# Optimization experiments

Measured on AMD Instinct MI355X. Metric: run time of the kernel, lower is better.

The kernel has to match this reference:

```python
import jax, jax.numpy as jnp
import numpy as np

B, T, HID = 2, 2048, 1024
H, DK, DV = 8, 128, 128      # num_heads, head_f_dim (key), head_i_dim (value)
LR = 128                     # gate low-rank dim
EPS = 1e-5


def setup_inputs() -> dict:
    key = jax.random.key(0)
    ks = jax.random.split(key, 8)
    def w(k, shape, fan_in):
        return jax.random.normal(k, shape, jnp.float32) / np.float32(np.sqrt(fan_in))
    return {
        "hidden_states": jax.random.normal(ks[0], (B, T, HID), jnp.float32),
        "Wq": w(ks[1], (HID, HID), HID),   # key_dim x hidden
        "Wk": w(ks[2], (HID, HID), HID),
        "Wv": w(ks[3], (HID, HID), HID),   # value_dim x hidden
        "Wg1": w(ks[4], (LR, HID), HID),   # low-rank gate down
        "Wg2": w(ks[5], (HID, LR), LR),    # low-rank gate up
        "g_norm_weight": jnp.ones((HID,), jnp.float32),
        "Wo": w(ks[6], (HID, HID), HID),
    }


def _lightnet_fwd(x, Wq, Wk, Wv, Wg1, Wg2, g_norm_weight, Wo):
    b, t, _ = x.shape
    q = jax.nn.silu(x @ Wq.T).reshape(b, t, H, DK)
    k = (x @ Wk.T).reshape(b, t, H, DK)
    v = (x @ Wv.T).reshape(b, t, H, DV)

    # LightNet gating: normalized keys via logcumsumexp over time
    z = jax.lax.cumlogsumexp(k, axis=1)                 # [b,t,h,dk]
    k = jnp.exp(k - z)                                  # exp-normalized keys
    g = jnp.concatenate([z[:, :1], z[:, :-1]], axis=1) - z  # <= 0; g[:,0]=0

    scale = DK ** -0.5

    # gated linear attention recurrence: S_t = exp(g_t) * S_{t-1} + k_t v_t^T
    def step(S, inp):
        qt, kt, vt, gt = inp                            # [b,h,dk],[b,h,dk],[b,h,dv],[b,h,dk]
        S = jnp.exp(gt)[..., None] * S + kt[..., None] * vt[..., None, :]
        o = jnp.einsum('bhk,bhkv->bhv', qt, S) * scale
        return S, o

    S0 = jnp.zeros((b, H, DK, DV), x.dtype)
    tfirst = lambda a: jnp.moveaxis(a, 1, 0)
    _, oT = jax.lax.scan(step, S0, (tfirst(q), tfirst(k), tfirst(v), tfirst(g)))
    o = jnp.moveaxis(oT, 0, 1).reshape(b, t, H * DV)    # [b,t,hidden]

    # RMSNorm(o) * swish(gate) then output projection
    gate = (x @ Wg1.T) @ Wg2.T
    o = o * jax.lax.rsqrt(jnp.mean(o * o, axis=-1, keepdims=True) + EPS) * g_norm_weight
    o = o * gate * jax.nn.sigmoid(gate)
    return o @ Wo.T


def reference(hidden_states, Wq, Wk, Wv, Wg1, Wg2, g_norm_weight, Wo):
    return _lightnet_fwd(hidden_states, Wq, Wk, Wv, Wg1, Wg2, g_norm_weight, Wo)
```

## Files before the change

kernel.cpp:

```cpp
#include <hip/hip_runtime.h>
#include <hip/hip_bf16.h>
#include <stdint.h>


typedef short short8 __attribute__((ext_vector_type(8)));
typedef float f32x4 __attribute__((ext_vector_type(4)));

#define T_SEQ 2048
#define HIDN  1024
#define SCALE 0.08838834764831845f
#define LDSP  136

__device__ __forceinline__ float blo(unsigned int u){
  union{unsigned int i; float f;} v; v.i = u << 16; return v.f;
}
__device__ __forceinline__ float bhi(unsigned int u){
  union{unsigned int i; float f;} v; v.i = u & 0xffff0000u; return v.f;
}
__device__ __forceinline__ float bu2f(unsigned short u){
  union{unsigned int i; float f;} v; v.i = ((unsigned int)u) << 16; return v.f;
}
__device__ __forceinline__ unsigned short f2bu(float f){
  union{float f; unsigned int i;} v; v.f = f;
  unsigned int x = v.i;
  x += 0x7fffu + ((x >> 16) & 1u);
  return (unsigned short)(x >> 16);
}
__device__ __forceinline__ void async16(const void* g, void* l){
  __builtin_amdgcn_global_load_lds(
      (const __attribute__((address_space(1))) unsigned int*)g,
      (__attribute__((address_space(3))) unsigned int*)l, 16, 0, 0);
}

__global__ __launch_bounds__(256) void convert_all(
    const float* __restrict__ X,  const float* __restrict__ Wq,
    const float* __restrict__ Wk, const float* __restrict__ Wv,
    const float* __restrict__ Wg1,const float* __restrict__ Wg2,
    const float* __restrict__ gnw,const float* __restrict__ Wo,
    unsigned short* __restrict__ base, float* __restrict__ SumSq)
{
  int q = blockIdx.x * 256 + threadIdx.x;
  const float* src; unsigned short* dst; int rel = q;
  if (rel < 1048576)            { src = X;   dst = base;            }
  else if ((rel -= 1048576) < 262144) { src = Wq;  dst = base + 4194304; }
  else if ((rel -=  262144) < 262144) { src = Wk;  dst = base + 5242880; }
  else if ((rel -=  262144) < 262144) { src = Wv;  dst = base + 6291456; }
  else if ((rel -=  262144) < 262144) { src = Wo;  dst = base + 7340032; }
  else if ((rel -=  262144) <  32768) { src = Wg1; dst = base + 8388608; }
  else if ((rel -=   32768) <  32768) { src = Wg2; dst = base + 8519680; }
  else if ((rel -=   32768) <    256) { src = gnw; dst = base + 8650752; }
  else { rel -= 256;
    ((float4*)SumSq)[rel] = make_float4(0.f,0.f,0.f,0.f); return; }
  float4 v = ((const float4*)src)[rel];
  ushort4 o; o.x=f2bu(v.x); o.y=f2bu(v.y); o.z=f2bu(v.z); o.w=f2bu(v.w);
  ((ushort4*)dst)[rel] = o;
}

__device__ __forceinline__ void gemm_core(
    const unsigned short* __restrict__ A, const unsigned short* __restrict__ B,
    int K, int row0, int col0,
    unsigned short* sA, unsigned short* sB, f32x4 acc[4][4], int tid)
{
  const int lane = tid & 63;
  const int wm = (tid >> 6) & 1, wn = tid >> 7;
  const int wb = tid & 192;
  for (int k0 = 0; k0 < K; k0 += 64){
    __syncthreads();
#pragma unroll
    for (int r = 0; r < 4; ++r){
      int idx  = r*256 + tid;
      int mrow = idx >> 3;
      int kc   = ((idx & 7) ^ (mrow & 7)) * 8;
      async16(A + (size_t)(row0 + mrow)*K + k0 + kc,
              sA + (size_t)(r*256 + wb)*8);
      async16(B + (size_t)(col0 + mrow)*K + k0 + kc,
              sB + (size_t)(r*256 + wb)*8);
    }
    __syncthreads();
#pragma unroll
    for (int h = 0; h < 2; ++h){
      short8 av[4], bv[4];
#pragma unroll
      for (int i=0;i<4;i++){
        int ra = wm*64 + i*16 + (lane&15);
        av[i] = *(const short8*)(sA + (size_t)ra*64
                                 + (((h*4 + (lane>>4)) ^ (ra & 7)) * 8));
      }
#pragma unroll
      for (int j=0;j<4;j++){
        int rb = wn*64 + j*16 + (lane&15);
        bv[j] = *(const short8*)(sB + (size_t)rb*64
                                 + (((h*4 + (lane>>4)) ^ (rb & 7)) * 8));
      }
#pragma unroll
      for (int i=0;i<4;i++)
#pragma unroll
        for (int j=0;j<4;j++)
          acc[i][j] = __builtin_amdgcn_mfma_f32_16x16x32_bf16(av[i], bv[j], acc[i][j], 0, 0, 0);
    }
  }
}

__device__ __forceinline__ void epilogue_lds(
    f32x4 acc[4][4], int row0, int col0, int tid, int ldc, int act,
    unsigned short* __restrict__ Cb, unsigned short* sC)
{
  const int lane = tid & 63;
  const int wm = (tid >> 6) & 1, wn = tid >> 7;
#pragma unroll
  for (int p=0;p<4;p++){
    __syncthreads();
    if (wm == (p>>1)){
#pragma unroll
      for (int ii=0; ii<2; ii++){
        int i = (p&1)*2 + ii;
        int lr = i*16 + ((lane>>4)<<2) - (p&1)*32;
#pragma unroll
        for (int j=0;j<4;j++){
          int col = wn*64 + j*16 + (lane&15);
#pragma unroll
          for (int r=0;r<4;r++){
            float v = acc[i][j][r];
            if (act == 1) v = v / (1.f + __expf(-v));
            else if (act == 2) v = __expf(v);
            sC[(lr+r)*128 + col] = f2bu(v);
          }
        }
      }
    }
    __syncthreads();
#pragma unroll
    for (int c = tid; c < 512; c += 256){
      int rr = c >> 4, off = (c & 15)*8;
      *(uint4*)&Cb[(size_t)(row0 + p*32 + rr)*ldc + col0 + off] =
          *(const uint4*)&sC[rr*128 + off];
    }
  }
}

__device__ __forceinline__ void epilogue_f32(
    f32x4 acc[4][4], int row0, int col0, int tid, int ldc,
    float* __restrict__ Cf)
{
  const int lane = tid & 63;
  const int wm = (tid >> 6) & 1, wn = tid >> 7;
#pragma unroll
  for (int i=0;i<4;i++){
    int rbase = row0 + wm*64 + i*16 + ((lane>>4)<<2);
#pragma unroll
    for (int j=0;j<4;j++){
      int col = col0 + wn*64 + j*16 + (lane&15);
#pragma unroll
      for (int r=0;r<4;r++)
        Cf[(size_t)(rbase + r)*ldc + col] = acc[i][j][r];
    }
  }
}

__device__ __forceinline__ void epilogue_vt(
    f32x4 acc[4][4], int row0, int col0, int tid,
    unsigned short* __restrict__ VT)
{
  const int lane = tid & 63, quad = lane >> 4, l15 = lane & 15;
  const int wm = (tid >> 6) & 1, wn = tid >> 7;
  size_t vtbase = ((size_t)(row0 >> 11)*8 + (col0 >> 7))*128;
  int trow0 = row0 & 2047;
#pragma unroll
  for (int i=0;i<4;i++){
    int t = trow0 + wm*64 + i*16 + quad*4;
#pragma unroll
    for (int j=0;j<4;j++){
      int v = wn*64 + j*16 + l15;
      ushort4 o;
      o.x = f2bu(acc[i][j][0]); o.y = f2bu(acc[i][j][1]);
      o.z = f2bu(acc[i][j][2]); o.w = f2bu(acc[i][j][3]);
      *(ushort4*)&VT[(vtbase + v)*2048 + t] = o;
    }
  }
}

__global__ __launch_bounds__(256, 4) void proj_kernel(
    const unsigned short* __restrict__ X,
    const unsigned short* __restrict__ Wq, const unsigned short* __restrict__ Wk,
    const unsigned short* __restrict__ Wv, const unsigned short* __restrict__ Wg1,
    unsigned short* __restrict__ Qb, unsigned short* __restrict__ Eb,
    unsigned short* __restrict__ VT, unsigned short* __restrict__ G1b)
{
  __shared__ unsigned short sA[128*64], sB[128*64];
  int tid = threadIdx.x;
  int which = blockIdx.y >> 3;
  const unsigned short* Bp = (which==0)?Wq:(which==1)?Wk:(which==2)?Wv:Wg1;
  int row0 = blockIdx.x * 128;
  int col0 = (which==3) ? 0 : (blockIdx.y & 7) * 128;
  f32x4 acc[4][4] = {};
  gemm_core(X, Bp, HIDN, row0, col0, sA, sB, acc, tid);
  if      (which==0) epilogue_lds(acc,row0,col0,tid,HIDN,1,Qb, sA);
  else if (which==1) epilogue_lds(acc,row0,col0,tid,HIDN,2,Eb, sA);
  else if (which==2) epilogue_vt (acc,row0,col0,tid,VT);
  else               epilogue_lds(acc,row0,col0,tid,128 ,0,G1b,sA);
}

__global__ __launch_bounds__(256, 4) void gemm_bt(
    const unsigned short* __restrict__ A, const unsigned short* __restrict__ B,
    int K, int ldc, int act, float* __restrict__ Cf,
    unsigned short* __restrict__ Cb)
{
  __shared__ unsigned short sA[128*64], sB[128*64];
  int tid = threadIdx.x;
  int row0 = blockIdx.x * 128, col0 = blockIdx.y * 128;
  f32x4 acc[4][4] = {};
  gemm_core(A, B, K, row0, col0, sA, sB, acc, tid);
  if (Cb) epilogue_lds(acc, row0, col0, tid, ldc, act, Cb, sA);
  else    epilogue_f32(acc, row0, col0, tid, ldc, Cf);
}

__device__ __forceinline__ void gemm_core64(
    const unsigned short* __restrict__ A, const unsigned short* __restrict__ B,
    int K, int row0, int col0,
    unsigned short* sA, unsigned short* sB, f32x4 acc[4][2], int tid)
{
  const int lane = tid & 63, quad = lane >> 4, l15 = lane & 15;
  const int wm = (tid >> 6) & 1, wn = tid >> 7;
  const int wb = tid & 192;
  for (int k0 = 0; k0 < K; k0 += 64){
    __syncthreads();
#pragma unroll
    for (int r = 0; r < 4; ++r){
      int idx  = r*256 + tid;
      int mrow = idx >> 3;
      int kc   = ((idx & 7) ^ (mrow & 7)) * 8;
      async16(A + (size_t)(row0 + mrow)*K + k0 + kc,
              sA + (size_t)(r*256 + wb)*8);
    }
#pragma unroll
    for (int r = 0; r < 2; ++r){
      int idx  = r*256 + tid;
      int brow = idx >> 3;
      int kc   = ((idx & 7) ^ (brow & 7)) * 8;
      async16(B + (size_t)(col0 + brow)*K + k0 + kc,
              sB + (size_t)(r*256 + wb)*8);
    }
    __syncthreads();
#pragma unroll
    for (int h = 0; h < 2; ++h){
      short8 av[4], bv[2];
#pragma unroll
      for (int i=0;i<4;i++){
        int ra = wm*64 + i*16 + l15;
        av[i] = *(const short8*)(sA + (size_t)ra*64
                                 + (((h*4 + quad) ^ (ra & 7)) * 8));
      }
#pragma unroll
      for (int j=0;j<2;j++){
        int rb = wn*32 + j*16 + l15;
        bv[j] = *(const short8*)(sB + (size_t)rb*64
                                 + (((h*4 + quad) ^ (rb & 7)) * 8));
      }
#pragma unroll
      for (int i=0;i<4;i++)
#pragma unroll
        for (int j=0;j<2;j++)
          acc[i][j] = __builtin_amdgcn_mfma_f32_16x16x32_bf16(av[i], bv[j], acc[i][j], 0, 0, 0);
    }
  }
}

__global__ __launch_bounds__(256, 4) void gemm_bt64(
    const unsigned short* __restrict__ A, const unsigned short* __restrict__ B,
    int K, int ldc, int act, float* __restrict__ Cf,
    unsigned short* __restrict__ Cb)
{
  __shared__ unsigned short sA[128*64], sB[64*64];
  int tid = threadIdx.x;
  const int lane = tid & 63, quad = lane >> 4, l15 = lane & 15;
  const int wm = (tid >> 6) & 1, wn = tid >> 7;
  int row0 = blockIdx.x * 128, col0 = blockIdx.y * 64;
  f32x4 acc[4][2] = {};
  gemm_core64(A, B, K, row0, col0, sA, sB, acc, tid);
  if (Cb){
    unsigned short* sC = sA;
#pragma unroll
    for (int p=0;p<4;p++){
      __syncthreads();
      if (wm == (p>>1)){
#pragma unroll
        for (int ii=0; ii<2; ii++){
          int i = (p&1)*2 + ii;
          int lr = i*16 + quad*4 - (p&1)*32;
#pragma unroll
          for (int j=0;j<2;j++){
            int col = wn*32 + j*16 + l15;
#pragma unroll
            for (int r=0;r<4;r++){
              float v = acc[i][j][r];
              if (act == 1) v = v / (1.f + __expf(-v));
              else if (act == 2) v = __expf(v);
              sC[(lr+r)*64 + col] = f2bu(v);
            }
          }
        }
      }
      __syncthreads();
      {
        int rr = tid >> 3, off = (tid & 7)*8;
        *(uint4*)&Cb[(size_t)(row0 + p*32 + rr)*ldc + col0 + off] =
            *(const uint4*)&sC[rr*64 + off];
      }
    }
  } else {
#pragma unroll
    for (int i=0;i<4;i++){
      int rbase = row0 + wm*64 + i*16 + quad*4;
#pragma unroll
      for (int j=0;j<2;j++){
        int col = col0 + wn*32 + j*16 + l15;
#pragma unroll
        for (int r=0;r<4;r++)
          Cf[(size_t)(rbase + r)*ldc + col] = acc[i][j][r];
      }
    }
  }
}

__global__ __launch_bounds__(1024, 2) void attn_pass1(
    const unsigned short* __restrict__ Eb, const unsigned short* __restrict__ VT,
    unsigned short* __restrict__ U, float* __restrict__ Esum)
{
  __shared__ unsigned short Vt[128*128];
  __shared__ unsigned short Et[128*LDSP];
  __shared__ float seg_part[8*128];
  int tid = threadIdx.x;
  const int lane = tid & 63, quad = lane >> 4, l15 = lane & 15;
  const int w = tid >> 6;
  const int Rb = (w & 3)*32, Cb = (w >> 2)*32;
  int bh = blockIdx.x >> 4, ch = blockIdx.x & 15;
  int b = bh >> 3, h = bh & 7;
  size_t rowbase = (size_t)(b*T_SEQ + ch*128)*HIDN + h*128;
  const unsigned short* VTb = VT + (size_t)bh*128*2048 + ch*128;

#pragma unroll
  for (int it=0; it<2; ++it){
    int slot = it*1024 + tid;
    int vrow = slot >> 4, c = slot & 15;
    int cs = (c & 8) | ((c & 7) ^ (vrow & 7));
    async16(VTb + (size_t)vrow*2048 + cs*8,
            Vt + (size_t)(it*1024 + (tid & 960))*8);
  }
#pragma unroll
  for (int i=0;i<2;i++){
    int u = tid + i*1024; int t = u >> 4, kc = (u & 15)*8;
    int trot = (t + kc) & 127;
    unsigned short tmp[8];
    *(uint4*)tmp = *(const uint4*)&Eb[rowbase + (size_t)t*HIDN + kc];
#pragma unroll
    for (int j=0;j<8;j++) Et[(kc+j)*LDSP + trot] = tmp[j];
  }
  __syncthreads();

  {
    int seg = tid >> 7, k = tid & 127;
    float s = 0.f;
    for (int c = seg*16; c < seg*16+16; ++c)
      s += bu2f(Et[k*LDSP + ((c + (k & 120)) & 127)]);
    seg_part[seg*128 + k] = s;
  }
  __syncthreads();
  if (tid < 128){
    float s = 0.f;
#pragma unroll
    for (int ss=0; ss<8; ++ss) s += seg_part[ss*128 + tid];
    Esum[(size_t)blockIdx.x*128 + tid] = s;
  }

  f32x4 acc[2][2] = {};
#pragma unroll
  for (int s0=0; s0<128; s0+=32){
    short8 av[2], bv[2];
#pragma unroll
    for (int i=0;i<2;i++){
      int ra = Rb + i*16 + l15;
      int ck = (s0>>3) + quad;
      int cx = (ck & 8) | ((ck & 7) ^ (ra & 7));
      av[i] = *(const short8*)(Vt + (size_t)ra*128 + cx*8);
    }
#pragma unroll
    for (int j=0;j<2;j++){
      int rb = Cb + j*16 + l15;
      bv[j] = *(const short8*)(Et + rb*LDSP + ((s0 + quad*8 + (rb & 120)) & 127));
    }
#pragma unroll
    for (int i=0;i<2;i++)
#pragma unroll
      for (int j=0;j<2;j++)
        acc[i][j] = __builtin_amdgcn_mfma_f32_16x16x32_bf16(av[i], bv[j], acc[i][j], 0,0,0);
  }
  __syncthreads();

#pragma unroll
  for (int i=0;i<2;i++)
#pragma unroll
    for (int j=0;j<2;j++){
      int k = Cb + j*16 + l15;
#pragma unroll
      for (int r=0;r<4;r++){
        int v = Rb + i*16 + quad*4 + r;
        Et[v*LDSP + k] = f2bu(acc[i][j][r]);
      }
    }
  __syncthreads();
  unsigned short* Ub = U + (size_t)blockIdx.x*16384;
#pragma unroll
  for (int i=0;i<2;i++){
    int u = tid + i*1024; int v = u >> 4, kc = (u & 15)*8;
    *(uint4*)&Ub[v*128 + kc] = *(const uint4*)&Et[v*LDSP + kc];
  }
}

__global__ __launch_bounds__(256) void attn_pass2(
    unsigned short* __restrict__ U, float* __restrict__ Esum)
{
  int bh = blockIdx.x >> 4, sl = blockIdx.x & 15;
  int p = sl*1024 + threadIdx.x*4;
  float r0=0.f, r1=0.f, r2=0.f, r3=0.f;
  for (int c=0;c<16;c++){
    ushort4* ptr = (ushort4*)&U[(size_t)(bh*16 + c)*16384 + p];
    ushort4 t = *ptr;
    ushort4 w;
    w.x=f2bu(r0); w.y=f2bu(r1); w.z=f2bu(r2); w.w=f2bu(r3);
    *ptr = w;
    r0 += bu2f(t.x); r1 += bu2f(t.y); r2 += bu2f(t.z); r3 += bu2f(t.w);
  }
  if (sl == 0 && threadIdx.x < 128){
    float r = 0.f;
    for (int c=0;c<16;c++){
      float* q = &Esum[(size_t)(bh*16 + c)*128 + threadIdx.x];
      float t = *q; *q = r; r += t;
    }
  }
}

__global__ __launch_bounds__(1024, 2) void attn_pass3(
    const unsigned short* __restrict__ Eb, const unsigned short* __restrict__ Qb,
    const unsigned short* __restrict__ VT, const unsigned short* __restrict__ U,
    const float* __restrict__ Esum, unsigned short* __restrict__ Oatt,
    float* __restrict__ SumSq)
{
  __shared__ unsigned short bufA[128*LDSP];
  __shared__ unsigned short bufB[128*LDSP];
  __shared__ float seg_part[8*128];

  int tid = threadIdx.x;
  const int lane = tid & 63, quad = lane >> 4, l15 = lane & 15;
  const int w = tid >> 6;
  const int Rb = (w & 3)*32;
  const int Cbn = (w >> 2)*32;
  int bh = blockIdx.x >> 4, ch = blockIdx.x & 15;
  int b = bh >> 3, h = bh & 7;
  size_t rowbase = (size_t)(b*T_SEQ + ch*128)*HIDN + h*128;
  const unsigned short* Ublk = U + (size_t)blockIdx.x*16384;
  const unsigned short* VTb = VT + (size_t)bh*128*2048 + ch*128;

#pragma unroll
  for (int i=0;i<2;i++){
    int u = tid + i*1024; int t = u >> 4, kc = (u & 15)*8;
    *(uint4*)&bufA[t*LDSP + kc] = *(const uint4*)&Qb[rowbase + (size_t)t*HIDN + kc];
    *(uint4*)&bufB[t*LDSP + kc] = *(const uint4*)&Eb[rowbase + (size_t)t*HIDN + kc];
  }
  __syncthreads();

  {
    int col = tid & 127, seg = tid >> 7;
    float psum = 0.f;
    for (int s = seg*16; s < seg*16+16; ++s) psum += bu2f(bufB[s*LDSP + col]);
    seg_part[seg*128 + col] = psum;
    __syncthreads();
    float run = Esum[(size_t)blockIdx.x*128 + col];
    for (int ss=0; ss<8; ++ss) if (ss < seg) run += seg_part[ss*128 + col];
    for (int s = seg*16; s < seg*16+16; ++s){
      run += bu2f(bufB[s*LDSP + col]);
      float q = bu2f(bufA[s*LDSP + col]);
      bufA[s*LDSP + col] = f2bu(q * SCALE * __builtin_amdgcn_rcpf(run));
    }
  }
  __syncthreads();

  f32x4 accO[2][2] = {}, accP[2][2] = {};
#pragma unroll
  for (int k0=0; k0<128; k0+=32){
    short8 av[2], uv[2], bv[2];
#pragma unroll
    for (int i=0;i<2;i++)
      av[i] = *(const short8*)(bufA + (Rb + i*16 + l15)*LDSP + k0 + quad*8);
#pragma unroll
    for (int j=0;j<2;j++)
      uv[j] = *(const short8*)(Ublk + (size_t)(Cbn + j*16 + l15)*128 + k0 + quad*8);
#pragma unroll
    for (int j=0;j<2;j++)
      bv[j] = *(const short8*)(bufB + (Cbn + j*16 + l15)*LDSP + k0 + quad*8);
#pragma unroll
    for (int i=0;i<2;i++)
#pragma unroll
      for (int j=0;j<2;j++)
        accP[i][j] = __builtin_amdgcn_mfma_f32_16x16x32_bf16(av[i], bv[j], accP[i][j], 0,0,0);
#pragma unroll
    for (int i=0;i<2;i++)
#pragma unroll
      for (int j=0;j<2;j++)
        accO[i][j] = __builtin_amdgcn_mfma_f32_16x16x32_bf16(av[i], uv[j], accO[i][j], 0,0,0);
  }
  __syncthreads();

#pragma unroll
  for (int it=0; it<2; ++it){
    int slot = it*1024 + tid;
    int vrow = slot >> 4, c = slot & 15;
    int cs = (c & 8) | ((c & 7) ^ (vrow & 7));
    async16(VTb + (size_t)vrow*2048 + cs*8,
            bufB + (size_t)(it*1024 + (tid & 960))*8);
  }
#pragma unroll
  for (int i=0;i<2;i++){
#pragma unroll
    for (int j=0;j<2;j++){
      int s = Cbn + j*16 + l15;
#pragma unroll
      for (int r=0;r<4;r++){
        int t = Rb + i*16 + quad*4 + r;
        bufA[t*LDSP + s] = f2bu(s <= t ? accP[i][j][r] : 0.f);
      }
    }
  }
  __syncthreads();

#pragma unroll
  for (int k0=0; k0<128; k0+=32){
    short8 av[2], bv[2];
#pragma unroll
    for (int i=0;i<2;i++)
      av[i] = *(const short8*)(bufA + (Rb + i*16 + l15)*LDSP + k0 + quad*8);
#pragma unroll
    for (int j=0;j<2;j++){
      int rv = Cbn + j*16 + l15;
      int ck = (k0>>3) + quad;
      int cx = (ck & 8) | ((ck & 7) ^ (rv & 7));
      bv[j] = *(const short8*)(bufB + (size_t)rv*128 + cx*8);
    }
#pragma unroll
    for (int i=0;i<2;i++)
#pragma unroll
      for (int j=0;j<2;j++)
        accO[i][j] = __builtin_amdgcn_mfma_f32_16x16x32_bf16(av[i], bv[j], accO[i][j], 0,0,0);
  }
  __syncthreads();

#pragma unroll
  for (int i=0;i<2;i++){
#pragma unroll
    for (int r=0;r<4;r++){
      int t = Rb + i*16 + quad*4 + r;
      float ss = 0.f;
#pragma unroll
      for (int j=0;j<2;j++){
        int vv = Cbn + j*16 + l15;
        unsigned short hb = f2bu(accO[i][j][r]);
        bufA[t*LDSP + vv] = hb;
        float xb = bu2f(hb); ss += xb*xb;
      }
      ss += __shfl_xor(ss, 1); ss += __shfl_xor(ss, 2);
      ss += __shfl_xor(ss, 4); ss += __shfl_xor(ss, 8);
      if (l15 == 0) seg_part[(w>>2)*128 + t] = ss;
    }
  }
  __syncthreads();

#pragma unroll
  for (int i=0;i<2;i++){
    int u = tid + i*1024; int t = u >> 4, kc = (u & 15)*8;
    *(uint4*)&Oatt[rowbase + (size_t)t*HIDN + kc] = *(const uint4*)&bufA[t*LDSP + kc];
  }
  if (tid < 128){
    float s = seg_part[tid] + seg_part[128+tid] + seg_part[256+tid] + seg_part[384+tid];
    atomicAdd(&SumSq[(size_t)b*T_SEQ + ch*128 + tid], s);
  }
}

__global__ __launch_bounds__(256) void norm_gate2(
    const unsigned short* __restrict__ Oatt, const unsigned short* __restrict__ Gt,
    const unsigned short* __restrict__ gnw, const float* __restrict__ SumSq,
    unsigned short* __restrict__ Onorm)
{
  int tid = threadIdx.x;
  int row = blockIdx.x*2 + (tid >> 7);
  int col = (tid & 127)*8;
  float rstd = rsqrtf(SumSq[row] * (1.f/1024.f) + 1e-5f);
  uint4 o4 = *(const uint4*)&Oatt[(size_t)row*HIDN + col];
  uint4 g4 = *(const uint4*)&Gt  [(size_t)row*HIDN + col];
  uint4 w4 = *(const uint4*)&gnw[col];
  auto mul2 = [&](unsigned int o, unsigned int g, unsigned int wv)->unsigned int{
    float lo = blo(o) * rstd * blo(wv) * blo(g);
    float hi = bhi(o) * rstd * bhi(wv) * bhi(g);
    return (unsigned int)f2bu(lo) | ((unsigned int)f2bu(hi) << 16);
  };
  uint4 r4;
  r4.x = mul2(o4.x, g4.x, w4.x); r4.y = mul2(o4.y, g4.y, w4.y);
  r4.z = mul2(o4.z, g4.z, w4.z); r4.w = mul2(o4.w, g4.w, w4.w);
  *(uint4*)&Onorm[(size_t)row*HIDN + col] = r4;
}

extern "C" void kernel_launch(void* const* d_in, const int* in_sizes, int n_in,
                              void* d_out, int out_size, void* d_ws, size_t ws_size,
                              hipStream_t stream) {
  unsigned short* wsS = (unsigned short*)d_ws;

  unsigned short* Xc   = wsS;
  unsigned short* Wqc  = wsS + 4194304;
  unsigned short* Wkc  = wsS + 5242880;
  unsigned short* Wvc  = wsS + 6291456;
  unsigned short* Woc  = wsS + 7340032;
  unsigned short* Wg1c = wsS + 8388608;
  unsigned short* Wg2c = wsS + 8519680;
  unsigned short* gnwc = wsS + 8650752;
  unsigned short* Qb   = wsS + 8651776;
  unsigned short* Eb   = wsS + 12846080;
  unsigned short* VTb  = wsS + 17040384;
  unsigned short* G1b  = wsS + 21234688;
  unsigned short* Gt   = wsS + 21758976;
  unsigned short* Ub   = wsS + 25953280;
  unsigned short* Oattb= wsS + 30147584;
  float*          Esum = (float*)(wsS + 34341888);
  float*          SumSq= (float*)(wsS + 34407424);
  unsigned short* Onorm = Qb;

  convert_all<<<8453, 256, 0, stream>>>(
      (const float*)d_in[0], (const float*)d_in[1], (const float*)d_in[2],
      (const float*)d_in[3], (const float*)d_in[4], (const float*)d_in[5],
      (const float*)d_in[6], (const float*)d_in[7], wsS, SumSq);

  proj_kernel<<<dim3(32,25), 256, 0, stream>>>(Xc, Wqc, Wkc, Wvc, Wg1c, Qb, Eb, VTb, G1b);
  gemm_bt64 <<<dim3(32,16), 256, 0, stream>>>(G1b, Wg2c, 128, HIDN, 1, nullptr, Gt);
  attn_pass1<<<256, 1024, 0, stream>>>(Eb, VTb, Ub, Esum);
  attn_pass2<<<256, 256, 0, stream>>>(Ub, Esum);
  attn_pass3<<<256, 1024, 0, stream>>>(Eb, Qb, VTb, Ub, Esum, Oattb, SumSq);
  norm_gate2<<<2048, 256, 0, stream>>>(Oattb, Gt, gnwc, SumSq, Onorm);
  gemm_bt64 <<<dim3(32,16), 256, 0, stream>>>(Onorm, Woc, HIDN, 1024, 0,
                                              (float*)d_out, nullptr);
}
```

Baseline: 188.1 us.

## Split attention pass1 over key halves and parallelize chunk prefix scan

Pass1 now runs 512 blocks of 512 threads, each handling half of the key dimension, and stages U output in the V tile buffer to use less shared memory. Pass2 switches from a serial 16-chunk scan to a two-level scan: 4 groups of 4 chunks each, combined through shared memory, launched over 1024 blocks. Pass3 reorders the two MFMA chains and computes the sum of squares with a separate LDS pass instead of shuffles. The aim is more parallelism and occupancy for the small scan kernels, in exchange for redundant V tile loads per key half and an extra barrier in pass3.

```diff
diff --git a/kernel.cpp b/kernel.cpp
--- a/kernel.cpp
+++ b/kernel.cpp
@@ -322,33 +322,35 @@
   }
 }
 
-__global__ __launch_bounds__(1024, 2) void attn_pass1(
+__global__ __launch_bounds__(512, 4) void attn_pass1(
     const unsigned short* __restrict__ Eb, const unsigned short* __restrict__ VT,
     unsigned short* __restrict__ U, float* __restrict__ Esum)
 {
   __shared__ unsigned short Vt[128*128];
-  __shared__ unsigned short Et[128*LDSP];
-  __shared__ float seg_part[8*128];
+  __shared__ unsigned short Et[64*LDSP];
+  __shared__ float seg_part[8*64];
   int tid = threadIdx.x;
   const int lane = tid & 63, quad = lane >> 4, l15 = lane & 15;
   const int w = tid >> 6;
-  const int Rb = (w & 3)*32, Cb = (w >> 2)*32;
-  int bh = blockIdx.x >> 4, ch = blockIdx.x & 15;
+  const int Rb = (w & 3)*32;
+  const int Cbk = (w >> 2)*32;
+  int bx = blockIdx.x;
+  int bh = bx >> 5, ch = (bx >> 1) & 15, kh = bx & 1;
   int b = bh >> 3, h = bh & 7;
-  size_t rowbase = (size_t)(b*T_SEQ + ch*128)*HIDN + h*128;
+  size_t rowbase = (size_t)(b*T_SEQ + ch*128)*HIDN + h*128 + kh*64;
   const unsigned short* VTb = VT + (size_t)bh*128*2048 + ch*128;
 
 #pragma unroll
-  for (int it=0; it<2; ++it){
-    int slot = it*1024 + tid;
+  for (int it=0; it<4; ++it){
+    int slot = it*512 + tid;
     int vrow = slot >> 4, c = slot & 15;
     int cs = (c & 8) | ((c & 7) ^ (vrow & 7));
     async16(VTb + (size_t)vrow*2048 + cs*8,
-            Vt + (size_t)(it*1024 + (tid & 960))*8);
+            Vt + (size_t)(it*512 + (tid & 448))*8);
   }
 #pragma unroll
   for (int i=0;i<2;i++){
-    int u = tid + i*1024; int t = u >> 4, kc = (u & 15)*8;
+    int u = tid + i*512; int t = u >> 3, kc = (u & 7)*8;
     int trot = (t + kc) & 127;
     unsigned short tmp[8];
     *(uint4*)tmp = *(const uint4*)&Eb[rowbase + (size_t)t*HIDN + kc];
@@ -358,18 +360,18 @@
   __syncthreads();
 
   {
-    int seg = tid >> 7, k = tid & 127;
+    int seg = tid >> 6, k = tid & 63;
     float s = 0.f;
     for (int c = seg*16; c < seg*16+16; ++c)
       s += bu2f(Et[k*LDSP + ((c + (k & 120)) & 127)]);
-    seg_part[seg*128 + k] = s;
-  }
-  __syncthreads();
-  if (tid < 128){
+    seg_part[seg*64 + k] = s;
+  }
+  __syncthreads();
+  if (tid < 64){
     float s = 0.f;
 #pragma unroll
-    for (int ss=0; ss<8; ++ss) s += seg_part[ss*128 + tid];
-    Esum[(size_t)blockIdx.x*128 + tid] = s;
+    for (int ss=0; ss<8; ++ss) s += seg_part[ss*64 + tid];
+    Esum[(size_t)(bh*16 + ch)*128 + kh*64 + tid] = s;
   }
 
   f32x4 acc[2][2] = {};
@@ -385,7 +387,7 @@
     }
 #pragma unroll
     for (int j=0;j<2;j++){
-      int rb = Cb + j*16 + l15;
+      int rb = Cbk + j*16 + l15;
       bv[j] = *(const short8*)(Et + rb*LDSP + ((s0 + quad*8 + (rb & 120)) & 127));
     }
 #pragma unroll
@@ -400,40 +402,61 @@
   for (int i=0;i<2;i++)
 #pragma unroll
     for (int j=0;j<2;j++){
-      int k = Cb + j*16 + l15;
+      int k = Cbk + j*16 + l15;
 #pragma unroll
       for (int r=0;r<4;r++){
         int v = Rb + i*16 + quad*4 + r;
-        Et[v*LDSP + k] = f2bu(acc[i][j][r]);
-      }
-    }
-  __syncthreads();
-  unsigned short* Ub = U + (size_t)blockIdx.x*16384;
+        Vt[v*64 + k] = f2bu(acc[i][j][r]);
+      }
+    }
+  __syncthreads();
+  unsigned short* Ub = U + (size_t)(bh*16 + ch)*16384;
 #pragma unroll
   for (int i=0;i<2;i++){
-    int u = tid + i*1024; int v = u >> 4, kc = (u & 15)*8;
-    *(uint4*)&Ub[v*128 + kc] = *(const uint4*)&Et[v*LDSP + kc];
+    int u = tid + i*512; int v = u >> 3, kc8 = (u & 7)*8;
+    *(uint4*)&Ub[v*128 + kh*64 + kc8] = *(const uint4*)&Vt[v*64 + kc8];
   }
 }
 
 __global__ __launch_bounds__(256) void attn_pass2(
     unsigned short* __restrict__ U, float* __restrict__ Esum)
 {
-  int bh = blockIdx.x >> 4, sl = blockIdx.x & 15;
-  int p = sl*1024 + threadIdx.x*4;
-  float r0=0.f, r1=0.f, r2=0.f, r3=0.f;
-  for (int c=0;c<16;c++){
-    ushort4* ptr = (ushort4*)&U[(size_t)(bh*16 + c)*16384 + p];
-    ushort4 t = *ptr;
-    ushort4 w;
-    w.x=f2bu(r0); w.y=f2bu(r1); w.z=f2bu(r2); w.w=f2bu(r3);
-    *ptr = w;
-    r0 += bu2f(t.x); r1 += bu2f(t.y); r2 += bu2f(t.z); r3 += bu2f(t.w);
-  }
-  if (sl == 0 && threadIdx.x < 128){
+  __shared__ float4 gs[4][64];
+  int tid = threadIdx.x;
+  int bh = blockIdx.x >> 6, slice = blockIdx.x & 63;
+  int pos = tid & 63, grp = tid >> 6;
+  size_t P4 = ((size_t)slice*64 + pos)*4;
+  ushort4 tv[4];
+#pragma unroll
+  for (int c=0;c<4;c++)
+    tv[c] = *(const ushort4*)&U[(size_t)(bh*16 + grp*4 + c)*16384 + P4];
+  float4 run = make_float4(0.f,0.f,0.f,0.f);
+  float4 excl[4];
+#pragma unroll
+  for (int c=0;c<4;c++){
+    excl[c] = run;
+    run.x += bu2f(tv[c].x); run.y += bu2f(tv[c].y);
+    run.z += bu2f(tv[c].z); run.w += bu2f(tv[c].w);
+  }
+  gs[grp][pos] = run;
+  __syncthreads();
+  float4 base = make_float4(0.f,0.f,0.f,0.f);
+  for (int g=0; g<grp; ++g){
+    float4 t = gs[g][pos];
+    base.x += t.x; base.y += t.y; base.z += t.z; base.w += t.w;
+  }
+#pragma unroll
+  for (int c=0;c<4;c++){
+    ushort4 w4;
+    w4.x = f2bu(base.x + excl[c].x); w4.y = f2bu(base.y + excl[c].y);
+    w4.z = f2bu(base.z + excl[c].z); w4.w = f2bu(base.w + excl[c].w);
+    *(ushort4*)&U[(size_t)(bh*16 + grp*4 + c)*16384 + P4] = w4;
+  }
+  if (slice < 2 && tid < 64){
+    int k = slice*64 + tid;
     float r = 0.f;
     for (int c=0;c<16;c++){
-      float* q = &Esum[(size_t)(bh*16 + c)*128 + threadIdx.x];
+      float* q = &Esum[(size_t)(bh*16 + c)*128 + k];
       float t = *q; *q = r; r += t;
     }
   }
@@ -487,13 +510,18 @@
   f32x4 accO[2][2] = {}, accP[2][2] = {};
 #pragma unroll
   for (int k0=0; k0<128; k0+=32){
-    short8 av[2], uv[2], bv[2];
+    short8 av[2], bv[2];
 #pragma unroll
     for (int i=0;i<2;i++)
       av[i] = *(const short8*)(bufA + (Rb + i*16 + l15)*LDSP + k0 + quad*8);
 #pragma unroll
     for (int j=0;j<2;j++)
-      uv[j] = *(const short8*)(Ublk + (size_t)(Cbn + j*16 + l15)*128 + k0 + quad*8);
+      bv[j] = *(const short8*)(Ublk + (size_t)(Cbn + j*16 + l15)*128 + k0 + quad*8);
+#pragma unroll
+    for (int i=0;i<2;i++)
+#pragma unroll
+      for (int j=0;j<2;j++)
+        accO[i][j] = __builtin_amdgcn_mfma_f32_16x16x32_bf16(av[i], bv[j], accO[i][j], 0,0,0);
 #pragma unroll
     for (int j=0;j<2;j++)
       bv[j] = *(const short8*)(bufB + (Cbn + j*16 + l15)*LDSP + k0 + quad*8);
@@ -502,11 +530,6 @@
 #pragma unroll
       for (int j=0;j<2;j++)
         accP[i][j] = __builtin_amdgcn_mfma_f32_16x16x32_bf16(av[i], bv[j], accP[i][j], 0,0,0);
-#pragma unroll
-    for (int i=0;i<2;i++)
-#pragma unroll
-      for (int j=0;j<2;j++)
-        accO[i][j] = __builtin_amdgcn_mfma_f32_16x16x32_bf16(av[i], uv[j], accO[i][j], 0,0,0);
   }
   __syncthreads();
 
@@ -556,30 +579,35 @@
 #pragma unroll
   for (int i=0;i<2;i++){
 #pragma unroll
-    for (int r=0;r<4;r++){
-      int t = Rb + i*16 + quad*4 + r;
-      float ss = 0.f;
-#pragma unroll
-      for (int j=0;j<2;j++){
-        int vv = Cbn + j*16 + l15;
-        unsigned short hb = f2bu(accO[i][j][r]);
-        bufA[t*LDSP + vv] = hb;
-        float xb = bu2f(hb); ss += xb*xb;
-      }
-      ss += __shfl_xor(ss, 1); ss += __shfl_xor(ss, 2);
-      ss += __shfl_xor(ss, 4); ss += __shfl_xor(ss, 8);
-      if (l15 == 0) seg_part[(w>>2)*128 + t] = ss;
-    }
-  }
-  __syncthreads();
-
+    for (int j=0;j<2;j++){
+      int vv = Cbn + j*16 + l15;
+#pragma unroll
+      for (int r=0;r<4;r++){
+        int t = Rb + i*16 + quad*4 + r;
+        bufA[t*LDSP + vv] = f2bu(accO[i][j][r]);
+      }
+    }
+  }
+  __syncthreads();
+
+  {
+    int seg = tid >> 7, row = tid & 127;
+    float s = 0.f;
+    for (int c = seg*16; c < seg*16+16; ++c){
+      float x = bu2f(bufA[row*LDSP + c]); s += x*x;
+    }
+    seg_part[seg*128 + row] = s;
+  }
 #pragma unroll
   for (int i=0;i<2;i++){
     int u = tid + i*1024; int t = u >> 4, kc = (u & 15)*8;
     *(uint4*)&Oatt[rowbase + (size_t)t*HIDN + kc] = *(const uint4*)&bufA[t*LDSP + kc];
   }
+  __syncthreads();
   if (tid < 128){
-    float s = seg_part[tid] + seg_part[128+tid] + seg_part[256+tid] + seg_part[384+tid];
+    float s = 0.f;
+#pragma unroll
+    for (int ss=0; ss<8; ++ss) s += seg_part[ss*128 + tid];
     atomicAdd(&SumSq[(size_t)b*T_SEQ + ch*128 + tid], s);
   }
 }
@@ -638,8 +666,8 @@
 
   proj_kernel<<<dim3(32,25), 256, 0, stream>>>(Xc, Wqc, Wkc, Wvc, Wg1c, Qb, Eb, VTb, G1b);
   gemm_bt64 <<<dim3(32,16), 256, 0, stream>>>(G1b, Wg2c, 128, HIDN, 1, nullptr, Gt);
-  attn_pass1<<<256, 1024, 0, stream>>>(Eb, VTb, Ub, Esum);
-  attn_pass2<<<256, 256, 0, stream>>>(Ub, Esum);
+  attn_pass1<<<512, 512, 0, stream>>>(Eb, VTb, Ub, Esum);
+  attn_pass2<<<1024, 256, 0, stream>>>(Ub, Esum);
   attn_pass3<<<256, 1024, 0, stream>>>(Eb, Qb, VTb, Ub, Esum, Oattb, SumSq);
   norm_gate2<<<2048, 256, 0, stream>>>(Oattb, Gt, gnwc, SumSq, Onorm);
   gemm_bt64 <<<dim3(32,16), 256, 0, stream>>>(Onorm, Woc, HIDN, 1024, 0,
```

Result: no change. 185.5 us (-1.4%).
